# Kernel optimization log

Hardware: AMD Instinct MI355X
Metric: run time of the kernel (lower is better)

Reference implementation:

```python
import jax, jax.numpy as jnp
import numpy as np

EPS = 1e-6


def setup_inputs() -> dict:
    key = jax.random.key(0)
    k1, k2, k3, k4, k5 = jax.random.split(key, 5)
    B, L, K, NFG, NH, NFO = 4, 1024, 32, 4, 16, 32
    return {
        "beta": jax.random.normal(k1, (B, L, NFG * NH), dtype=jnp.float32),
        "self_attention": jax.random.normal(k2, (B, L, NFG * NH), dtype=jnp.float32),
        "attn_coef": jax.random.normal(k3, (B, L, K, NFG * NH), dtype=jnp.float32),
        "node_out": jax.random.normal(k4, (B, L, K, NFO * NH), dtype=jnp.float32),
        "graph_weights": jax.random.uniform(k5, (B, L, K, NFG), dtype=jnp.float32),
    }


def reference(beta, self_attention, attn_coef, node_out, graph_weights):
    B, L, K, nfg = graph_weights.shape
    nh = attn_coef.shape[-1] // nfg
    nfo = node_out.shape[-1] // nh

    beta = beta.reshape(B, L, nfg, nh)
    sa = self_attention.reshape(B, L, nfg, nh)
    ac = attn_coef.reshape(B, L, K, nfg, nh)
    no = node_out.reshape(B, L, K, nfo, nh)

    # add self-attention term to the first (self) neighbor slot
    ac = ac.at[:, :, 0].add(sa)
    # beta gating, broadcast over neighbors
    ac = ac * (beta[:, :, None] + EPS)
    # stabilized exp over (K, nfg) jointly
    ac = ac - jnp.max(ac, axis=(-3, -2), keepdims=True)
    weighted = jnp.exp(ac) * graph_weights[..., None]          # [B,L,K,nfg,nh]
    attn_final = jnp.sum(weighted, axis=-2)                    # [B,L,K,nh]
    attn_final = attn_final / (jnp.sum(jnp.abs(attn_final), axis=-2, keepdims=True) + EPS)
    # weighted aggregation over neighbors
    output = jnp.einsum("blkfh,blkh->blfh", no, attn_final).reshape(B, L, nfo * nh)
    return output, attn_final
```

## Files before the change

kernel.cpp:

```cpp
#include <hip/hip_runtime.h>

#define EPS 1e-6f

constexpr int KNB = 32;
constexpr int NFG = 4;
constexpr int NH  = 16;
constexpr int NFO = 32;
constexpr int FH  = NFG * NH;
constexpr int ACN = KNB * FH;
constexpr int ON  = NFO * NH;
constexpr int KN  = KNB * NH;

__global__ __launch_bounds__(256)
void attn_fused(const float* __restrict__ beta,
                const float* __restrict__ sa,
                const float* __restrict__ ac,
                const float* __restrict__ no,
                const float* __restrict__ gw,
                float* __restrict__ out,
                float* __restrict__ attn_out)
{
    const int bl  = blockIdx.x;
    const int tid = threadIdx.x;

    __shared__ float s_ac[ACN];
    __shared__ float s_attn[KN];
    __shared__ float s_gw[KNB * NFG];
    __shared__ float s_bg[FH];
    __shared__ float s_red[256];
    __shared__ float s_m[NH];
    __shared__ float s_d[NH];

    const size_t blz = (size_t)bl;
    const float* acp = ac + blz * ACN;
    const float* nop = no + blz * (size_t)(KNB * ON);
    const float* gwp = gw + blz * (KNB * NFG);

    if (tid < FH) s_bg[tid] = beta[blz * FH + tid] + EPS;
    if (tid < KNB * NFG) s_gw[tid] = gwp[tid];
    __syncthreads();

    const int h = tid & 15;

    float lmax = -INFINITY;
    #pragma unroll
    for (int j = 0; j < 8; ++j) {
        const int idx = tid + j * 256;
        const int k   = idx >> 6;
        const int fh  = idx & 63;
        float v = acp[idx];
        if (k == 0) v += sa[blz * FH + fh];
        v *= s_bg[fh];
        s_ac[idx] = v;
        lmax = fmaxf(lmax, v);
    }

    s_red[tid] = lmax;
    __syncthreads();
    if (tid < 128) s_red[tid] = fmaxf(s_red[tid], s_red[tid + 128]);
    __syncthreads();
    if (tid < 64)  s_red[tid] = fmaxf(s_red[tid], s_red[tid + 64]);
    __syncthreads();
    if (tid < 32)  s_red[tid] = fmaxf(s_red[tid], s_red[tid + 32]);
    __syncthreads();
    if (tid < 16)  s_m[tid]   = fmaxf(s_red[tid], s_red[tid + 16]);
    __syncthreads();

    const float m = s_m[h];
    const int k0 = tid >> 4;
    const int k1 = k0 + 16;
    float a0 = 0.f, a1 = 0.f;
    #pragma unroll
    for (int f = 0; f < NFG; ++f) {
        a0 += expf(s_ac[k0 * 64 + f * 16 + h] - m) * s_gw[k0 * 4 + f];
        a1 += expf(s_ac[k1 * 64 + f * 16 + h] - m) * s_gw[k1 * 4 + f];
    }

    __syncthreads();
    s_red[tid] = fabsf(a0) + fabsf(a1);
    __syncthreads();
    if (tid < 128) s_red[tid] += s_red[tid + 128];
    __syncthreads();
    if (tid < 64)  s_red[tid] += s_red[tid + 64];
    __syncthreads();
    if (tid < 32)  s_red[tid] += s_red[tid + 32];
    __syncthreads();
    if (tid < 16)  s_d[tid]   = s_red[tid] + s_red[tid + 16];
    __syncthreads();

    const float den = s_d[h] + EPS;
    const float n0 = a0 / den;
    const float n1 = a1 / den;
    s_attn[tid]        = n0;
    s_attn[tid + 256]  = n1;
    attn_out[blz * KN + tid]       = n0;
    attn_out[blz * KN + tid + 256] = n1;
    __syncthreads();

    const int i2 = tid * 2;
    const int h0 = i2 & 15;
    float accx = 0.f, accy = 0.f;
    #pragma unroll
    for (int k = 0; k < KNB; ++k) {
        const float2 v = *reinterpret_cast<const float2*>(nop + k * ON + i2);
        accx += v.x * s_attn[k * NH + h0];
        accy += v.y * s_attn[k * NH + h0 + 1];
    }
    float2 r; r.x = accx; r.y = accy;
    *reinterpret_cast<float2*>(out + blz * ON + i2) = r;
}

extern "C" void kernel_launch(void* const* d_in, const int* in_sizes, int n_in,
                              void* d_out, int out_size, void* d_ws, size_t ws_size,
                              hipStream_t stream) {
    const float* beta = (const float*)d_in[0];
    const float* sa   = (const float*)d_in[1];
    const float* ac   = (const float*)d_in[2];
    const float* no   = (const float*)d_in[3];
    const float* gw   = (const float*)d_in[4];

    const int BL = in_sizes[0] / FH;
    float* out      = (float*)d_out;
    float* attn_out = out + (size_t)BL * ON;

    attn_fused<<<BL, 256, 0, stream>>>(beta, sa, ac, no, gw, out, attn_out);
}
```

Baseline: 389.1 us.

## Use wave shuffles for reductions and float4 split-K aggregation

Replaces the multi-stage shared-memory tree reductions for the max and the abs-sum with wave-level xor shuffles plus a single cross-wave combine, removing several block barriers. The final neighbor aggregation now uses float4 loads, with the 32 neighbors split between two halves of the block and combined through shared memory. It also switches to fast __expf and adds an occupancy hint to launch bounds. The extra partial-sum buffer and barrier add some shared memory, and __expf slightly changes numerics.

```diff
diff --git a/kernel.cpp b/kernel.cpp
--- a/kernel.cpp
+++ b/kernel.cpp
@@ -11,7 +11,7 @@
 constexpr int ON  = NFO * NH;
 constexpr int KN  = KNB * NH;
 
-__global__ __launch_bounds__(256)
+__global__ __launch_bounds__(256, 4)
 void attn_fused(const float* __restrict__ beta,
                 const float* __restrict__ sa,
                 const float* __restrict__ ac,
@@ -20,24 +20,25 @@
                 float* __restrict__ out,
                 float* __restrict__ attn_out)
 {
-    const int bl  = blockIdx.x;
-    const int tid = threadIdx.x;
+    const int bl   = blockIdx.x;
+    const int tid  = threadIdx.x;
+    const int lane = tid & 63;
+    const int wv   = tid >> 6;
 
     __shared__ float s_ac[ACN];
     __shared__ float s_attn[KN];
     __shared__ float s_gw[KNB * NFG];
     __shared__ float s_bg[FH];
-    __shared__ float s_red[256];
-    __shared__ float s_m[NH];
-    __shared__ float s_d[NH];
+    __shared__ float s_wm[4 * NH];
+    __shared__ float s_wd[4 * NH];
+    __shared__ float s_part[ON];
 
     const size_t blz = (size_t)bl;
     const float* acp = ac + blz * ACN;
     const float* nop = no + blz * (size_t)(KNB * ON);
-    const float* gwp = gw + blz * (KNB * NFG);
 
-    if (tid < FH) s_bg[tid] = beta[blz * FH + tid] + EPS;
-    if (tid < KNB * NFG) s_gw[tid] = gwp[tid];
+    if (tid < FH)        s_bg[tid] = beta[blz * FH + tid] + EPS;
+    if (tid < KNB * NFG) s_gw[tid] = gw[blz * (KNB * NFG) + tid];
     __syncthreads();
 
     const int h = tid & 15;
@@ -46,68 +47,67 @@
     #pragma unroll
     for (int j = 0; j < 8; ++j) {
         const int idx = tid + j * 256;
-        const int k   = idx >> 6;
-        const int fh  = idx & 63;
         float v = acp[idx];
-        if (k == 0) v += sa[blz * FH + fh];
-        v *= s_bg[fh];
+        if (j == 0 && tid < FH) v += sa[blz * FH + tid];
+        v *= s_bg[idx & 63];
         s_ac[idx] = v;
         lmax = fmaxf(lmax, v);
     }
 
-    s_red[tid] = lmax;
+    lmax = fmaxf(lmax, __shfl_xor(lmax, 16, 64));
+    lmax = fmaxf(lmax, __shfl_xor(lmax, 32, 64));
+    if (lane < 16) s_wm[wv * 16 + lane] = lmax;
     __syncthreads();
-    if (tid < 128) s_red[tid] = fmaxf(s_red[tid], s_red[tid + 128]);
-    __syncthreads();
-    if (tid < 64)  s_red[tid] = fmaxf(s_red[tid], s_red[tid + 64]);
-    __syncthreads();
-    if (tid < 32)  s_red[tid] = fmaxf(s_red[tid], s_red[tid + 32]);
-    __syncthreads();
-    if (tid < 16)  s_m[tid]   = fmaxf(s_red[tid], s_red[tid + 16]);
-    __syncthreads();
+    const float m = fmaxf(fmaxf(s_wm[h], s_wm[16 + h]),
+                          fmaxf(s_wm[32 + h], s_wm[48 + h]));
 
-    const float m = s_m[h];
     const int k0 = tid >> 4;
-    const int k1 = k0 + 16;
     float a0 = 0.f, a1 = 0.f;
     #pragma unroll
     for (int f = 0; f < NFG; ++f) {
-        a0 += expf(s_ac[k0 * 64 + f * 16 + h] - m) * s_gw[k0 * 4 + f];
-        a1 += expf(s_ac[k1 * 64 + f * 16 + h] - m) * s_gw[k1 * 4 + f];
+        a0 += __expf(s_ac[k0 * 64 + f * 16 + h] - m)        * s_gw[k0 * 4 + f];
+        a1 += __expf(s_ac[(k0 + 16) * 64 + f * 16 + h] - m) * s_gw[(k0 + 16) * 4 + f];
     }
 
+    float ls = fabsf(a0) + fabsf(a1);
+    ls += __shfl_xor(ls, 16, 64);
+    ls += __shfl_xor(ls, 32, 64);
+    if (lane < 16) s_wd[wv * 16 + lane] = ls;
     __syncthreads();
-    s_red[tid] = fabsf(a0) + fabsf(a1);
-    __syncthreads();
-    if (tid < 128) s_red[tid] += s_red[tid + 128];
-    __syncthreads();
-    if (tid < 64)  s_red[tid] += s_red[tid + 64];
-    __syncthreads();
-    if (tid < 32)  s_red[tid] += s_red[tid + 32];
-    __syncthreads();
-    if (tid < 16)  s_d[tid]   = s_red[tid] + s_red[tid + 16];
-    __syncthreads();
+    const float den = s_wd[h] + s_wd[16 + h] + s_wd[32 + h] + s_wd[48 + h] + EPS;
 
-    const float den = s_d[h] + EPS;
     const float n0 = a0 / den;
     const float n1 = a1 / den;
-    s_attn[tid]        = n0;
-    s_attn[tid + 256]  = n1;
+    s_attn[tid]       = n0;
+    s_attn[tid + 256] = n1;
     attn_out[blz * KN + tid]       = n0;
     attn_out[blz * KN + tid + 256] = n1;
     __syncthreads();
 
-    const int i2 = tid * 2;
-    const int h0 = i2 & 15;
-    float accx = 0.f, accy = 0.f;
-    #pragma unroll
-    for (int k = 0; k < KNB; ++k) {
-        const float2 v = *reinterpret_cast<const float2*>(nop + k * ON + i2);
-        accx += v.x * s_attn[k * NH + h0];
-        accy += v.y * s_attn[k * NH + h0 + 1];
+    const int half = tid >> 7;
+    const int u    = tid & 127;
+    const int p    = u * 4;
+    const float* basep = nop + half * ON + p;
+    float4 acc = make_float4(0.f, 0.f, 0.f, 0.f);
+    #pragma unroll 8
+    for (int j = 0; j < 16; ++j) {
+        const float4 v = *reinterpret_cast<const float4*>(basep + j * 1024);
+        const float4 w = *reinterpret_cast<const float4*>(
+            &s_attn[(2 * j + half) * 16 + (p & 15)]);
+        acc.x += v.x * w.x;
+        acc.y += v.y * w.y;
+        acc.z += v.z * w.z;
+        acc.w += v.w * w.w;
     }
-    float2 r; r.x = accx; r.y = accy;
-    *reinterpret_cast<float2*>(out + blz * ON + i2) = r;
+    if (half) {
+        *reinterpret_cast<float4*>(&s_part[p]) = acc;
+    }
+    __syncthreads();
+    if (!half) {
+        const float4 q = *reinterpret_cast<const float4*>(&s_part[p]);
+        acc.x += q.x; acc.y += q.y; acc.z += q.z; acc.w += q.w;
+        *reinterpret_cast<float4*>(out + blz * ON + p) = acc;
+    }
 }
 
 extern "C" void kernel_launch(void* const* d_in, const int* in_sizes, int n_in,
```

New measurement: 387.2 us. About the same (-0.5%).
